# Kernel tuning notes

Hardware: AMD Instinct MI355X
Metric: run time of the kernel (lower is better)

The kernel has to match this reference:

```python
import jax, jax.numpy as jnp
import numpy as np

TOP_K = 8
NEG_SLOPE = 0.2  # PyG GATConv default negative_slope


def setup_inputs() -> dict:
    key = jax.random.key(0)
    ks = jax.random.split(key, 8)
    B, C, T, D, H, KD = 16, 64, 128, 256, 8, 32
    s = 1.0 / np.sqrt(D)
    return {
        "x": jax.random.normal(ks[0], (B, C, T, D), jnp.float32),
        "static_adj": jax.random.normal(ks[1], (C, C), jnp.float32),
        "w_q": jax.random.normal(ks[2], (KD, D), jnp.float32) * s,
        "w_k": jax.random.normal(ks[3], (KD, D), jnp.float32) * s,
        "gat_lin": jax.random.normal(ks[4], (H * D, D), jnp.float32) * s,  # shared lin_src/lin_dst
        "att_src": jax.random.normal(ks[5], (H, D), jnp.float32) * s,
        "att_dst": jax.random.normal(ks[6], (H, D), jnp.float32) * s,
        "gat_bias": jnp.zeros((D,), jnp.float32),
    }


def reference(x, static_adj, w_q, w_k, gat_lin, att_src, att_dst, gat_bias):
    B, C, T, D = x.shape
    H = att_src.shape[0]
    kd = w_q.shape[0]

    # ---- dynamic adjacency ----
    h = x.mean(axis=2)                                   # [B,C,D] temporal summary
    q = h @ w_q.T                                        # [B,C,KD]
    k = h @ w_k.T                                        # [B,C,KD]
    sim = jnp.einsum('bik,bjk->bij', q, k) / np.float32(np.sqrt(kd))
    delta_a = jnp.tanh(sim)                              # [B,C,C]
    adaptive = static_adj[None] + delta_a                # [B,C,C]

    # top-k per row -> sparse mask (edge: row i = source, col j = target, per dense_to_sparse)
    _, idx = jax.lax.top_k(jnp.abs(adaptive), TOP_K)     # [B,C,K]
    mask = jnp.any(jax.nn.one_hot(idx, C, dtype=bool), axis=-2)  # [B,C,C]
    mask = mask | jnp.eye(C, dtype=bool)                 # GATConv add_self_loops=True

    # ---- GAT message passing (dense masked attention, graph shared across T) ----
    xt = jnp.swapaxes(x, 1, 2)                           # [B,T,C,D]
    wx = (xt @ gat_lin.T).reshape(B, T, C, H, D)         # [B,T,C,H,F]
    a_s = jnp.einsum('btchf,hf->btch', wx, att_src)      # source term
    a_d = jnp.einsum('btchf,hf->btch', wx, att_dst)      # target term
    # e[b,t,i,j,h]: edge source i -> target j
    e = a_s[:, :, :, None, :] + a_d[:, :, None, :, :]
    e = jax.nn.leaky_relu(e, NEG_SLOPE)
    e = jnp.where(mask[:, None, :, :, None], e, -jnp.inf)
    alpha = jax.nn.softmax(e, axis=2)                    # softmax over incoming sources i per target j
    out = jnp.einsum('btijh,btihf->btjhf', alpha, wx)    # aggregate messages
    out = out.mean(axis=3) + gat_bias                    # concat=False -> mean heads, add bias
    x_updated = jnp.swapaxes(out, 1, 2)                  # [B,C,T,D]
    return x_updated, delta_a
```

## Files before the change

kernel.cpp:

```cpp
#include <hip/hip_runtime.h>

typedef _Float16 h2_t __attribute__((ext_vector_type(2)));
typedef _Float16 h4_t __attribute__((ext_vector_type(4)));
typedef _Float16 h8_t __attribute__((ext_vector_type(8)));
typedef __fp16 fp16x2 __attribute__((ext_vector_type(2)));
typedef float f32x16 __attribute__((ext_vector_type(16)));


__device__ __forceinline__ h2_t pkrtz(float a, float b) {
  union { fp16x2 f; h2_t h; } u;
  u.f = __builtin_amdgcn_cvt_pkrtz(a, b);
  return u.h;
}

__device__ __forceinline__ float fdot2_(h2_t a, h2_t b, float c) {
#if __has_builtin(__builtin_amdgcn_fdot2)
  return __builtin_amdgcn_fdot2(a, b, c, false);
#else
  return fmaf((float)a[0], (float)b[0], fmaf((float)a[1], (float)b[1], c));
#endif
}

__device__ __forceinline__ h2_t u2h(unsigned u) {
  union { unsigned u; h2_t h; } x; x.u = u; return x.h;
}

__device__ __forceinline__ void gload16(const void* g, void* l) {
  __builtin_amdgcn_global_load_lds(
      (const __attribute__((address_space(1))) void*)g,
      (__attribute__((address_space(3))) void*)l, 16, 0, 0);
}

__global__ void k_hmean(const float* __restrict__ x, float* __restrict__ h) {
  int bc = blockIdx.x;
  int d = threadIdx.x;
  const float* xp = x + (size_t)bc * (128 * 256) + d;
  float s = 0.f;
  #pragma unroll 8
  for (int t = 0; t < 128; ++t) s += xp[(size_t)t * 256];
  h[bc * 256 + d] = s * (1.f / 128.f);
}

__global__ void k_qk(const float* __restrict__ h, const float* __restrict__ wq,
                     const float* __restrict__ wk, float* __restrict__ q,
                     float* __restrict__ k) {
  int gid = blockIdx.x * 256 + threadIdx.x;
  int isK = gid >> 15;
  int e = gid & 32767;
  int kk = e & 31;
  int bi = e >> 5;
  const float4* h4 = (const float4*)(h + bi * 256);
  const float4* w4 = (const float4*)((isK ? wk : wq) + kk * 256);
  float s = 0.f;
  #pragma unroll 4
  for (int d = 0; d < 64; ++d) {
    float4 a = h4[d], bv = w4[d];
    s = fmaf(a.x, bv.x, s); s = fmaf(a.y, bv.y, s);
    s = fmaf(a.z, bv.z, s); s = fmaf(a.w, bv.w, s);
  }
  (isK ? k : q)[e] = s;
}

__global__ void k_adj(const float* __restrict__ q, const float* __restrict__ k,
                      const float* __restrict__ sadj, float* __restrict__ dout,
                      unsigned long long* __restrict__ cmask) {
  __shared__ float qs[64][33], ks[64][33];
  __shared__ float ad[64][65];
  __shared__ unsigned long long rowm[64];
  int b = blockIdx.x, tid = threadIdx.x;
  for (int r = 0; r < 8; ++r) {
    int idx = r * 256 + tid;
    qs[idx >> 5][idx & 31] = q[b * 2048 + idx];
    ks[idx >> 5][idx & 31] = k[b * 2048 + idx];
  }
  __syncthreads();
  const float rs = 0.17677669529663687f;
  for (int r = 0; r < 16; ++r) {
    int idx = r * 256 + tid;
    int i = idx >> 6, j = idx & 63;
    float s = 0.f;
    #pragma unroll 8
    for (int kk = 0; kk < 32; ++kk) s = fmaf(qs[i][kk], ks[j][kk], s);
    float dv = tanhf(s * rs);
    dout[b * 4096 + idx] = dv;
    ad[i][j] = sadj[idx] + dv;
  }
  __syncthreads();
  if (tid < 64) {
    unsigned long long sel = 0ull;
    for (int p = 0; p < 8; ++p) {
      float best = -1.f; int bj = 0;
      for (int j = 0; j < 64; ++j) {
        if ((sel >> j) & 1ull) continue;
        float v = fabsf(ad[tid][j]);
        if (v > best) { best = v; bj = j; }
      }
      sel |= 1ull << bj;
    }
    rowm[tid] = sel;
  }
  __syncthreads();
  if (tid < 64) {
    unsigned long long cmv = 1ull << tid;
    for (int i = 0; i < 64; ++i) cmv |= ((rowm[i] >> tid) & 1ull) << i;
    cmask[b * 64 + tid] = cmv;
  }
}

__global__ void k_vsd(const float* __restrict__ glin, const float* __restrict__ asrc,
                      const float* __restrict__ adst, _Float16* __restrict__ vsd16) {
  int hh = blockIdx.x, d = threadIdx.x;
  const float* gb = glin + (size_t)hh * 65536;
  float s = 0.f, t = 0.f;
  for (int f = 0; f < 256; ++f) {
    float g = gb[f * 256 + d];
    s = fmaf(asrc[hh * 256 + f], g, s);
    t = fmaf(adst[hh * 256 + f], g, t);
  }
  vsd16[hh * 256 + d] = (_Float16)s;
  vsd16[(8 + hh) * 256 + d] = (_Float16)t;
}

__global__ void k_gswz(const float* __restrict__ g, _Float16* __restrict__ o) {
  int gid = blockIdx.x * 256 + threadIdx.x;
  int s = gid & 7;
  int f = (gid >> 3) & 255;
  int sc = gid >> 11;
  int h = sc >> 2, dc = sc & 3;
  const float* src = g + ((size_t)(h * 256 + f) << 8) + dc * 64 + (((s ^ (f & 7)) & 7) << 3);
  float4 a = *(const float4*)src;
  float4 bq = *(const float4*)(src + 4);
  h8_t v;
  v[0] = (_Float16)a.x;  v[1] = (_Float16)a.y;  v[2] = (_Float16)a.z;  v[3] = (_Float16)a.w;
  v[4] = (_Float16)bq.x; v[5] = (_Float16)bq.y; v[6] = (_Float16)bq.z; v[7] = (_Float16)bq.w;
  *(h8_t*)(o + (size_t)gid * 8) = v;
}

__global__ __launch_bounds__(512) void k_main(
    const float* __restrict__ x, const _Float16* __restrict__ vsd16,
    const unsigned long long* __restrict__ cmask,
    const _Float16* __restrict__ g16s, const float* __restrict__ bias,
    float* __restrict__ out)
{
  __shared__ __align__(16) char LDS[143360];
  char* XR  = LDS;
  char* GB  = LDS + 32768;
  char* WXT = LDS + 98304;
  char* PT  = LDS + 131072;
  float* AS = (float*)(LDS + 139264);
  float* AD = (float*)(LDS + 141312);

  const int tid = threadIdx.x;
  const int lane = tid & 63;
  const int w = __builtin_amdgcn_readfirstlane(tid >> 6);
  const int hi = lane >> 5;
  const int l5 = lane & 31;
  const int l7 = lane & 7;
  const int mg = w & 1;
  const int fg = w >> 1;
  const int bt = blockIdx.x;
  const int b = bt >> 7, t = bt & 127;

  const int jj = w * 8 + (lane >> 3);
  const unsigned long long cm = cmask[b * 64 + jj];
  const int fb0 = l5 + fg * 64, fb1 = fb0 + 32;
  const float bi0 = bias[fb0], bi1 = bias[fb1];

  {
    const char* gs = (const char*)g16s + (size_t)w * 4096 + (size_t)lane * 16;
    char* ld = GB + w * 4096;
    #pragma unroll
    for (int q = 0; q < 4; ++q) gload16(gs + q * 1024, ld + q * 1024);
  }

  #pragma unroll
  for (int r = 0; r < 8; ++r) {
    int i = w * 8 + r;
    const float4 v = *(const float4*)(x + (((size_t)(b * 64 + i) * 128 + t) << 8) + lane * 4);
    h2_t p0 = pkrtz(v.x, v.y);
    h2_t p1 = pkrtz(v.z, v.w);
    h4_t hv; hv[0] = p0[0]; hv[1] = p0[1]; hv[2] = p1[0]; hv[3] = p1[1];
    int db = lane >> 1;
    int off = i * 512 + (((db & 24) | ((db ^ (i & 7)) & 7)) << 4) + ((lane & 1) << 3);
    *(h4_t*)(XR + off) = hv;
  }
  asm volatile("s_waitcnt vmcnt(0)" ::: "memory");
  asm volatile("s_waitcnt lgkmcnt(0)" ::: "memory");
  __builtin_amdgcn_s_barrier();

  h8_t Af[16];
  {
    int i = mg * 32 + l5;
    #pragma unroll
    for (int k = 0; k < 16; ++k) {
      int db = k * 2 + hi;
      Af[k] = *(const h8_t*)(XR + i * 512 + (((db & 24) | ((db ^ l7) & 7)) << 4));
    }
  }

  {
    float a_s = 0.f, a_d = 0.f;
    const unsigned* vsp = (const unsigned*)vsd16 + w * 128;
    const unsigned* vdp = (const unsigned*)vsd16 + (8 + w) * 128;
    #pragma unroll 4
    for (int db = 0; db < 32; ++db) {
      h8_t xv = *(const h8_t*)(XR + lane * 512 + (((db & 24) | ((db ^ l7) & 7)) << 4));
      #pragma unroll
      for (int c = 0; c < 4; ++c) {
        h2_t x2; x2[0] = xv[c * 2]; x2[1] = xv[c * 2 + 1];
        a_s = fdot2_(x2, u2h(vsp[db * 4 + c]), a_s);
        a_d = fdot2_(x2, u2h(vdp[db * 4 + c]), a_d);
      }
    }
    AS[w * 64 + lane] = a_s;
    AD[w * 64 + lane] = a_d;
  }
  asm volatile("s_waitcnt lgkmcnt(0)" ::: "memory");
  __builtin_amdgcn_s_barrier();

  f32x16 acc00 = {}, acc01 = {}, acc10 = {}, acc11 = {};

  #pragma unroll 1
  for (int h = 0; h < 8; ++h) {
    f32x16 d0 = {}, d1 = {};
    #pragma unroll
    for (int dc = 0; dc < 4; ++dc) {
      const int s = h * 4 + dc;
      asm volatile("s_waitcnt lgkmcnt(0)" ::: "memory");
      __builtin_amdgcn_s_barrier();
      if (s < 31) {
        const char* gs = (const char*)g16s + (size_t)(s + 1) * 32768 + (size_t)w * 4096 + (size_t)lane * 16;
        char* ld = GB + ((s + 1) & 1) * 32768 + w * 4096;
        #pragma unroll
        for (int q = 0; q < 4; ++q) gload16(gs + q * 1024, ld + q * 1024);
        asm volatile("s_waitcnt vmcnt(4)" ::: "memory");
      } else {
        asm volatile("s_waitcnt vmcnt(0)" ::: "memory");
      }
      __builtin_amdgcn_s_barrier();

      if (dc == 0) {
        const int ip = lane & 7;
        float ad_j = AD[h * 64 + jj];
        float ev[8], m = -1e30f;
        #pragma unroll
        for (int c = 0; c < 8; ++c) {
          int i = ip * 8 + c;
          float e = AS[h * 64 + i] + ad_j;
          e = (e > 0.f) ? e : 0.2f * e;
          e = ((cm >> i) & 1ULL) ? e : -1e30f;
          ev[c] = e; m = fmaxf(m, e);
        }
        m = fmaxf(m, __shfl_xor(m, 1));
        m = fmaxf(m, __shfl_xor(m, 2));
        m = fmaxf(m, __shfl_xor(m, 4));
        float ss = 0.f;
        #pragma unroll
        for (int c = 0; c < 8; ++c) { ev[c] = __expf(ev[c] - m); ss += ev[c]; }
        ss += __shfl_xor(ss, 1); ss += __shfl_xor(ss, 2); ss += __shfl_xor(ss, 4);
        float rinv = 1.f / ss;
        h8_t pv;
        #pragma unroll
        for (int c = 0; c < 4; ++c) {
          h2_t p = pkrtz(ev[2 * c] * rinv, ev[2 * c + 1] * rinv);
          pv[2 * c] = p[0]; pv[2 * c + 1] = p[1];
        }
        *(h8_t*)(PT + jj * 128 + (((ip ^ (jj & 7)) & 7) << 4)) = pv;
      }

      const char* gb = GB + (s & 1) * 32768;
      #pragma unroll
      for (int kk = 0; kk < 4; ++kk) {
        int sl = (((kk * 2 + hi) ^ l7) & 7) << 4;
        h8_t b0 = *(const h8_t*)(gb + fb0 * 128 + sl);
        h8_t b1 = *(const h8_t*)(gb + fb1 * 128 + sl);
        d0 = __builtin_amdgcn_mfma_f32_32x32x16_f16(Af[dc * 4 + kk], b0, d0, 0, 0, 0);
        d1 = __builtin_amdgcn_mfma_f32_32x32x16_f16(Af[dc * 4 + kk], b1, d1, 0, 0, 0);
      }
    }

    #pragma unroll
    for (int rq = 0; rq < 4; ++rq) {
      int db = mg * 4 + rq;
      int sl = ((db ^ l7) & 7) << 4;
      h2_t a0 = pkrtz(d0[rq * 4 + 0], d0[rq * 4 + 1]);
      h2_t a1 = pkrtz(d0[rq * 4 + 2], d0[rq * 4 + 3]);
      h4_t v0; v0[0] = a0[0]; v0[1] = a0[1]; v0[2] = a1[0]; v0[3] = a1[1];
      *(h4_t*)(WXT + fb0 * 128 + sl + hi * 8) = v0;
      h2_t b0p = pkrtz(d1[rq * 4 + 0], d1[rq * 4 + 1]);
      h2_t b1p = pkrtz(d1[rq * 4 + 2], d1[rq * 4 + 3]);
      h4_t v1; v1[0] = b0p[0]; v1[1] = b0p[1]; v1[2] = b1p[0]; v1[3] = b1p[1];
      *(h4_t*)(WXT + fb1 * 128 + sl + hi * 8) = v1;
    }
    asm volatile("s_waitcnt lgkmcnt(0)" ::: "memory");
    __builtin_amdgcn_s_barrier();

    #pragma unroll
    for (int kb = 0; kb < 4; ++kb) {
      int sl = (((kb * 2 + hi) ^ l7) & 7) << 4;
      h8_t pa0 = *(const h8_t*)(PT + l5 * 128 + sl);
      h8_t pa1 = *(const h8_t*)(PT + (l5 + 32) * 128 + sl);
      h8_t wb0 = *(const h8_t*)(WXT + fb0 * 128 + sl);
      h8_t wb1 = *(const h8_t*)(WXT + fb1 * 128 + sl);
      acc00 = __builtin_amdgcn_mfma_f32_32x32x16_f16(pa0, wb0, acc00, 0, 0, 0);
      acc01 = __builtin_amdgcn_mfma_f32_32x32x16_f16(pa0, wb1, acc01, 0, 0, 0);
      acc10 = __builtin_amdgcn_mfma_f32_32x32x16_f16(pa1, wb0, acc10, 0, 0, 0);
      acc11 = __builtin_amdgcn_mfma_f32_32x32x16_f16(pa1, wb1, acc11, 0, 0, 0);
    }
  }

  float* ob = out + ((size_t)(b * 64) * 128 + t) * 256;
  #pragma unroll
  for (int rq = 0; rq < 4; ++rq) {
    #pragma unroll
    for (int rr = 0; rr < 4; ++rr) {
      int r = rq * 4 + rr;
      int j0 = 8 * rq + 4 * hi + rr;
      ob[(size_t)j0 * 32768 + fb0]        = acc00[r] * 0.125f + bi0;
      ob[(size_t)j0 * 32768 + fb1]        = acc01[r] * 0.125f + bi1;
      ob[(size_t)(j0 + 32) * 32768 + fb0] = acc10[r] * 0.125f + bi0;
      ob[(size_t)(j0 + 32) * 32768 + fb1] = acc11[r] * 0.125f + bi1;
    }
  }
}

extern "C" void kernel_launch(void* const* d_in, const int* in_sizes, int n_in,
                              void* d_out, int out_size, void* d_ws, size_t ws_size,
                              hipStream_t stream) {
  const float* x    = (const float*)d_in[0];
  const float* sadj = (const float*)d_in[1];
  const float* wq   = (const float*)d_in[2];
  const float* wk   = (const float*)d_in[3];
  const float* glin = (const float*)d_in[4];
  const float* asrc = (const float*)d_in[5];
  const float* adst = (const float*)d_in[6];
  const float* bias = (const float*)d_in[7];

  float* out = (float*)d_out;
  float* delta_out = out + (size_t)16 * 64 * 128 * 256;

  char* ws = (char*)d_ws;
  float* h   = (float*)(ws + 0);
  float* q   = (float*)(ws + 1048576);
  float* k   = (float*)(ws + 1179648);
  unsigned long long* cm = (unsigned long long*)(ws + 1310720);
  _Float16* vsd16 = (_Float16*)(ws + 1318912);
  _Float16* g16s  = (_Float16*)(ws + 1327104);

  hipLaunchKernelGGL(k_hmean, dim3(1024), dim3(256), 0, stream, x, h);
  hipLaunchKernelGGL(k_qk,    dim3(256),  dim3(256), 0, stream, h, wq, wk, q, k);
  hipLaunchKernelGGL(k_adj,   dim3(16),   dim3(256), 0, stream, q, k, sadj, delta_out, cm);
  hipLaunchKernelGGL(k_vsd,   dim3(8),    dim3(256), 0, stream, glin, asrc, adst, vsd16);
  hipLaunchKernelGGL(k_gswz,  dim3(256),  dim3(256), 0, stream, glin, g16s);
  hipLaunchKernelGGL(k_main,  dim3(2048), dim3(512), 0, stream, x, vsd16, cm, g16s, bias, out);
}
```

Baseline: 373.4 us.

## Keep GAT weights and wx in registers, split aggregation K across wave pairs

Drops the LDS double-buffered weight staging. Each wave now loads pre-rearranged fp16 gat_lin fragments straight from global memory into registers, double-buffered as GA/GB. The wx tile is repacked in registers through lane shuffles instead of a round trip through LDS, and the softmax is precomputed once per (head, target) as a log-sum-exp offset, so attention weights are built directly in registers. The aggregation K dimension is split across the two mg wave groups and combined through an LDS reduction at the end. This removes most per-step barriers and cuts LDS use, in exchange for more register pressure and redundant global weight loads per wave.

Result: slower. 419.0 us (+12.2%).

```diff
diff --git a/kernel.cpp b/kernel.cpp
--- a/kernel.cpp
+++ b/kernel.cpp
@@ -11,6 +11,18 @@
   union { fp16x2 f; h2_t h; } u;
   u.f = __builtin_amdgcn_cvt_pkrtz(a, b);
   return u.h;
+}
+
+__device__ __forceinline__ unsigned pk_u(float a, float b) {
+  union { fp16x2 f; unsigned u; } z;
+  z.f = __builtin_amdgcn_cvt_pkrtz(a, b);
+  return z.u;
+}
+
+__device__ __forceinline__ h8_t mk8(unsigned w0, unsigned w1, unsigned w2, unsigned w3) {
+  union { unsigned u[4]; h8_t h; } z;
+  z.u[0] = w0; z.u[1] = w1; z.u[2] = w2; z.u[3] = w3;
+  return z.h;
 }
 
 __device__ __forceinline__ float fdot2_(h2_t a, h2_t b, float c) {
@@ -23,12 +35,6 @@
 
 __device__ __forceinline__ h2_t u2h(unsigned u) {
   union { unsigned u; h2_t h; } x; x.u = u; return x.h;
-}
-
-__device__ __forceinline__ void gload16(const void* g, void* l) {
-  __builtin_amdgcn_global_load_lds(
-      (const __attribute__((address_space(1))) void*)g,
-      (__attribute__((address_space(3))) void*)l, 16, 0, 0);
 }
 
 __global__ void k_hmean(const float* __restrict__ x, float* __restrict__ h) {
@@ -121,13 +127,17 @@
   vsd16[(8 + hh) * 256 + d] = (_Float16)t;
 }
 
-__global__ void k_gswz(const float* __restrict__ g, _Float16* __restrict__ o) {
+__global__ void k_grearr(const float* __restrict__ g, _Float16* __restrict__ o) {
   int gid = blockIdx.x * 256 + threadIdx.x;
-  int s = gid & 7;
-  int f = (gid >> 3) & 255;
-  int sc = gid >> 11;
-  int h = sc >> 2, dc = sc & 3;
-  const float* src = g + ((size_t)(h * 256 + f) << 8) + dc * 64 + (((s ^ (f & 7)) & 7) << 3);
+  int lane = gid & 63;
+  int fg = (gid >> 6) & 3;
+  int FID = gid >> 8;
+  int ft = FID & 1, kk = (FID >> 1) & 3, s = FID >> 3;
+  int h = s >> 2, dc = s & 3;
+  int l5 = lane & 31, hi = lane >> 5;
+  int f = fg * 64 + ft * 32 + l5;
+  int d0 = dc * 64 + kk * 16 + hi * 8;
+  const float* src = g + ((size_t)(h * 256 + f) << 8) + d0;
   float4 a = *(const float4*)src;
   float4 bq = *(const float4*)(src + 4);
   h8_t v;
@@ -139,16 +149,15 @@
 __global__ __launch_bounds__(512) void k_main(
     const float* __restrict__ x, const _Float16* __restrict__ vsd16,
     const unsigned long long* __restrict__ cmask,
-    const _Float16* __restrict__ g16s, const float* __restrict__ bias,
+    const _Float16* __restrict__ g16r, const float* __restrict__ bias,
     float* __restrict__ out)
 {
-  __shared__ __align__(16) char LDS[143360];
-  char* XR  = LDS;
-  char* GB  = LDS + 32768;
-  char* WXT = LDS + 98304;
-  char* PT  = LDS + 131072;
-  float* AS = (float*)(LDS + 139264);
-  float* AD = (float*)(LDS + 141312);
+  __shared__ __align__(16) char LDS[106496];
+  char* XR   = LDS;
+  float* ASp = (float*)(LDS + 32768);
+  float* ADp = (float*)(LDS + 34816);
+  float* OFFp= (float*)(LDS + 36864);
+  char* RED  = LDS + 40960;
 
   const int tid = threadIdx.x;
   const int lane = tid & 63;
@@ -161,17 +170,19 @@
   const int bt = blockIdx.x;
   const int b = bt >> 7, t = bt & 127;
 
-  const int jj = w * 8 + (lane >> 3);
-  const unsigned long long cm = cmask[b * 64 + jj];
-  const int fb0 = l5 + fg * 64, fb1 = fb0 + 32;
-  const float bi0 = bias[fb0], bi1 = bias[fb1];
-
-  {
-    const char* gs = (const char*)g16s + (size_t)w * 4096 + (size_t)lane * 16;
-    char* ld = GB + w * 4096;
-    #pragma unroll
-    for (int q = 0; q < 4; ++q) gload16(gs + q * 1024, ld + q * 1024);
-  }
+  const char* gb0 = (const char*)g16r + fg * 1024 + lane * 16;
+
+  h8_t GA[8], GB[8];
+  #pragma unroll
+  for (int q = 0; q < 8; ++q) GA[q] = *(const h8_t*)(gb0 + q * 4096);
+
+  const unsigned long long cm0 = cmask[b * 64 + l5];
+  const unsigned long long cm1 = cmask[b * 64 + 32 + l5];
+  const int shb = mg * 32 + hi * 8;
+  const unsigned mb00 = (unsigned)(cm0 >> shb)        & 0xffu;
+  const unsigned mb01 = (unsigned)(cm0 >> (shb + 16)) & 0xffu;
+  const unsigned mb10 = (unsigned)(cm1 >> shb)        & 0xffu;
+  const unsigned mb11 = (unsigned)(cm1 >> (shb + 16)) & 0xffu;
 
   #pragma unroll
   for (int r = 0; r < 8; ++r) {
@@ -184,9 +195,7 @@
     int off = i * 512 + (((db & 24) | ((db ^ (i & 7)) & 7)) << 4) + ((lane & 1) << 3);
     *(h4_t*)(XR + off) = hv;
   }
-  asm volatile("s_waitcnt vmcnt(0)" ::: "memory");
-  asm volatile("s_waitcnt lgkmcnt(0)" ::: "memory");
-  __builtin_amdgcn_s_barrier();
+  __syncthreads();
 
   h8_t Af[16];
   {
@@ -212,115 +221,174 @@
         a_d = fdot2_(x2, u2h(vdp[db * 4 + c]), a_d);
       }
     }
-    AS[w * 64 + lane] = a_s;
-    AD[w * 64 + lane] = a_d;
+    ASp[w * 64 + lane] = a_s;
+    ADp[w * 64 + lane] = a_d;
   }
   asm volatile("s_waitcnt lgkmcnt(0)" ::: "memory");
-  __builtin_amdgcn_s_barrier();
+
+  {
+    const int j = lane;
+    const unsigned long long cmj = cmask[b * 64 + j];
+    const float adj = ADp[w * 64 + j];
+    float m = -1e30f;
+    #pragma unroll 8
+    for (int i = 0; i < 64; ++i) {
+      float e = ASp[w * 64 + i] + adj;
+      e = fmaxf(e, 0.f) + 0.2f * fminf(e, 0.f);
+      e = ((cmj >> i) & 1ull) ? e : -1e30f;
+      m = fmaxf(m, e);
+    }
+    float ssum = 0.f;
+    #pragma unroll 8
+    for (int i = 0; i < 64; ++i) {
+      float e = ASp[w * 64 + i] + adj;
+      e = fmaxf(e, 0.f) + 0.2f * fminf(e, 0.f);
+      e = ((cmj >> i) & 1ull) ? e : -1e30f;
+      ssum += exp2f((e - m) * 1.44269504f);
+    }
+    OFFp[w * 64 + j] = fmaf(-1.44269504f, m, -log2f(ssum));
+  }
+  __syncthreads();
 
   f32x16 acc00 = {}, acc01 = {}, acc10 = {}, acc11 = {};
 
   #pragma unroll 1
   for (int h = 0; h < 8; ++h) {
     f32x16 d0 = {}, d1 = {};
+
     #pragma unroll
     for (int dc = 0; dc < 4; ++dc) {
       const int s = h * 4 + dc;
-      asm volatile("s_waitcnt lgkmcnt(0)" ::: "memory");
-      __builtin_amdgcn_s_barrier();
-      if (s < 31) {
-        const char* gs = (const char*)g16s + (size_t)(s + 1) * 32768 + (size_t)w * 4096 + (size_t)lane * 16;
-        char* ld = GB + ((s + 1) & 1) * 32768 + w * 4096;
-        #pragma unroll
-        for (int q = 0; q < 4; ++q) gload16(gs + q * 1024, ld + q * 1024);
-        asm volatile("s_waitcnt vmcnt(4)" ::: "memory");
+      const int sp = (s < 31) ? s + 1 : 31;
+      const char* gpp = gb0 + (size_t)sp * 32768;
+      if ((dc & 1) == 0) {
+        #pragma unroll
+        for (int q = 0; q < 8; ++q) GB[q] = *(const h8_t*)(gpp + q * 4096);
+        #pragma unroll
+        for (int kk = 0; kk < 4; ++kk) {
+          d0 = __builtin_amdgcn_mfma_f32_32x32x16_f16(Af[dc * 4 + kk], GA[kk * 2 + 0], d0, 0, 0, 0);
+          d1 = __builtin_amdgcn_mfma_f32_32x32x16_f16(Af[dc * 4 + kk], GA[kk * 2 + 1], d1, 0, 0, 0);
+        }
       } else {
-        asm volatile("s_waitcnt vmcnt(0)" ::: "memory");
-      }
-      __builtin_amdgcn_s_barrier();
-
-      if (dc == 0) {
-        const int ip = lane & 7;
-        float ad_j = AD[h * 64 + jj];
-        float ev[8], m = -1e30f;
-        #pragma unroll
-        for (int c = 0; c < 8; ++c) {
-          int i = ip * 8 + c;
-          float e = AS[h * 64 + i] + ad_j;
-          e = (e > 0.f) ? e : 0.2f * e;
-          e = ((cm >> i) & 1ULL) ? e : -1e30f;
-          ev[c] = e; m = fmaxf(m, e);
-        }
-        m = fmaxf(m, __shfl_xor(m, 1));
-        m = fmaxf(m, __shfl_xor(m, 2));
-        m = fmaxf(m, __shfl_xor(m, 4));
-        float ss = 0.f;
-        #pragma unroll
-        for (int c = 0; c < 8; ++c) { ev[c] = __expf(ev[c] - m); ss += ev[c]; }
-        ss += __shfl_xor(ss, 1); ss += __shfl_xor(ss, 2); ss += __shfl_xor(ss, 4);
-        float rinv = 1.f / ss;
-        h8_t pv;
-        #pragma unroll
-        for (int c = 0; c < 4; ++c) {
-          h2_t p = pkrtz(ev[2 * c] * rinv, ev[2 * c + 1] * rinv);
-          pv[2 * c] = p[0]; pv[2 * c + 1] = p[1];
-        }
-        *(h8_t*)(PT + jj * 128 + (((ip ^ (jj & 7)) & 7) << 4)) = pv;
-      }
-
-      const char* gb = GB + (s & 1) * 32768;
+        #pragma unroll
+        for (int q = 0; q < 8; ++q) GA[q] = *(const h8_t*)(gpp + q * 4096);
+        #pragma unroll
+        for (int kk = 0; kk < 4; ++kk) {
+          d0 = __builtin_amdgcn_mfma_f32_32x32x16_f16(Af[dc * 4 + kk], GB[kk * 2 + 0], d0, 0, 0, 0);
+          d1 = __builtin_amdgcn_mfma_f32_32x32x16_f16(Af[dc * 4 + kk], GB[kk * 2 + 1], d1, 0, 0, 0);
+        }
+      }
+    }
+
+    h8_t B2[2][2];
+    {
+      const bool H = (hi != 0);
       #pragma unroll
-      for (int kk = 0; kk < 4; ++kk) {
-        int sl = (((kk * 2 + hi) ^ l7) & 7) << 4;
-        h8_t b0 = *(const h8_t*)(gb + fb0 * 128 + sl);
-        h8_t b1 = *(const h8_t*)(gb + fb1 * 128 + sl);
-        d0 = __builtin_amdgcn_mfma_f32_32x32x16_f16(Af[dc * 4 + kk], b0, d0, 0, 0, 0);
-        d1 = __builtin_amdgcn_mfma_f32_32x32x16_f16(Af[dc * 4 + kk], b1, d1, 0, 0, 0);
-      }
-    }
-
+      for (int ft = 0; ft < 2; ++ft) {
+        const f32x16& dd = ft ? d1 : d0;
+        unsigned P0 = pk_u(dd[0], dd[1]),  P1 = pk_u(dd[2], dd[3]);
+        unsigned P2 = pk_u(dd[4], dd[5]),  P3 = pk_u(dd[6], dd[7]);
+        unsigned P4 = pk_u(dd[8], dd[9]),  P5 = pk_u(dd[10], dd[11]);
+        unsigned P6 = pk_u(dd[12], dd[13]), P7 = pk_u(dd[14], dd[15]);
+        {
+          unsigned Pa = H ? P2 : P0, Pb = H ? P3 : P1;
+          unsigned Qa = H ? P0 : P2, Qb = H ? P1 : P3;
+          unsigned S0 = (unsigned)__shfl_xor((int)Qa, 32);
+          unsigned S1 = (unsigned)__shfl_xor((int)Qb, 32);
+          B2[0][ft] = mk8(H ? S0 : Pa, H ? S1 : Pb, H ? Pa : S0, H ? Pb : S1);
+        }
+        {
+          unsigned Pa = H ? P6 : P4, Pb = H ? P7 : P5;
+          unsigned Qa = H ? P4 : P6, Qb = H ? P5 : P7;
+          unsigned S0 = (unsigned)__shfl_xor((int)Qa, 32);
+          unsigned S1 = (unsigned)__shfl_xor((int)Qb, 32);
+          B2[1][ft] = mk8(H ? S0 : Pa, H ? S1 : Pb, H ? Pa : S0, H ? Pb : S1);
+        }
+      }
+    }
+
+    const float adj0 = ADp[h * 64 + l5];
+    const float adj1 = ADp[h * 64 + 32 + l5];
+    const float off0 = OFFp[h * 64 + l5];
+    const float off1 = OFFp[h * 64 + 32 + l5];
+    const float* asp = ASp + h * 64 + mg * 32 + hi * 8;
+    float4 asA0 = *(const float4*)(asp);
+    float4 asA1 = *(const float4*)(asp + 4);
+    float4 asB0 = *(const float4*)(asp + 16);
+    float4 asB1 = *(const float4*)(asp + 20);
+    float asv[2][8];
+    asv[0][0]=asA0.x; asv[0][1]=asA0.y; asv[0][2]=asA0.z; asv[0][3]=asA0.w;
+    asv[0][4]=asA1.x; asv[0][5]=asA1.y; asv[0][6]=asA1.z; asv[0][7]=asA1.w;
+    asv[1][0]=asB0.x; asv[1][1]=asB0.y; asv[1][2]=asB0.z; asv[1][3]=asB0.w;
+    asv[1][4]=asB1.x; asv[1][5]=asB1.y; asv[1][6]=asB1.z; asv[1][7]=asB1.w;
+
+    h8_t A2[2][2];
     #pragma unroll
-    for (int rq = 0; rq < 4; ++rq) {
-      int db = mg * 4 + rq;
-      int sl = ((db ^ l7) & 7) << 4;
-      h2_t a0 = pkrtz(d0[rq * 4 + 0], d0[rq * 4 + 1]);
-      h2_t a1 = pkrtz(d0[rq * 4 + 2], d0[rq * 4 + 3]);
-      h4_t v0; v0[0] = a0[0]; v0[1] = a0[1]; v0[2] = a1[0]; v0[3] = a1[1];
-      *(h4_t*)(WXT + fb0 * 128 + sl + hi * 8) = v0;
-      h2_t b0p = pkrtz(d1[rq * 4 + 0], d1[rq * 4 + 1]);
-      h2_t b1p = pkrtz(d1[rq * 4 + 2], d1[rq * 4 + 3]);
-      h4_t v1; v1[0] = b0p[0]; v1[1] = b0p[1]; v1[2] = b1p[0]; v1[3] = b1p[1];
-      *(h4_t*)(WXT + fb1 * 128 + sl + hi * 8) = v1;
-    }
-    asm volatile("s_waitcnt lgkmcnt(0)" ::: "memory");
-    __builtin_amdgcn_s_barrier();
-
+    for (int jt = 0; jt < 2; ++jt) {
+      const float adj = jt ? adj1 : adj0;
+      const float off = jt ? off1 : off0;
+      #pragma unroll
+      for (int kbl = 0; kbl < 2; ++kbl) {
+        const unsigned mb = jt ? (kbl ? mb11 : mb10) : (kbl ? mb01 : mb00);
+        float vv[8];
+        #pragma unroll
+        for (int e = 0; e < 8; ++e) {
+          float ee = asv[kbl][e] + adj;
+          ee = fmaxf(ee, 0.f) + 0.2f * fminf(ee, 0.f);
+          ee = ((mb >> e) & 1u) ? ee : -1e30f;
+          vv[e] = exp2f(fmaf(ee, 1.44269504f, off));
+        }
+        A2[jt][kbl] = mk8(pk_u(vv[0], vv[1]), pk_u(vv[2], vv[3]),
+                          pk_u(vv[4], vv[5]), pk_u(vv[6], vv[7]));
+      }
+    }
+
+    acc00 = __builtin_amdgcn_mfma_f32_32x32x16_f16(A2[0][0], B2[0][0], acc00, 0, 0, 0);
+    acc00 = __builtin_amdgcn_mfma_f32_32x32x16_f16(A2[0][1], B2[1][0], acc00, 0, 0, 0);
+    acc01 = __builtin_amdgcn_mfma_f32_32x32x16_f16(A2[0][0], B2[0][1], acc01, 0, 0, 0);
+    acc01 = __builtin_amdgcn_mfma_f32_32x32x16_f16(A2[0][1], B2[1][1], acc01, 0, 0, 0);
+    acc10 = __builtin_amdgcn_mfma_f32_32x32x16_f16(A2[1][0], B2[0][0], acc10, 0, 0, 0);
+    acc10 = __builtin_amdgcn_mfma_f32_32x32x16_f16(A2[1][1], B2[1][0], acc10, 0, 0, 0);
+    acc11 = __builtin_amdgcn_mfma_f32_32x32x16_f16(A2[1][0], B2[0][1], acc11, 0, 0, 0);
+    acc11 = __builtin_amdgcn_mfma_f32_32x32x16_f16(A2[1][1], B2[1][1], acc11, 0, 0, 0);
+  }
+
+  if (mg == 1) {
     #pragma unroll
-    for (int kb = 0; kb < 4; ++kb) {
-      int sl = (((kb * 2 + hi) ^ l7) & 7) << 4;
-      h8_t pa0 = *(const h8_t*)(PT + l5 * 128 + sl);
-      h8_t pa1 = *(const h8_t*)(PT + (l5 + 32) * 128 + sl);
-      h8_t wb0 = *(const h8_t*)(WXT + fb0 * 128 + sl);
-      h8_t wb1 = *(const h8_t*)(WXT + fb1 * 128 + sl);
-      acc00 = __builtin_amdgcn_mfma_f32_32x32x16_f16(pa0, wb0, acc00, 0, 0, 0);
-      acc01 = __builtin_amdgcn_mfma_f32_32x32x16_f16(pa0, wb1, acc01, 0, 0, 0);
-      acc10 = __builtin_amdgcn_mfma_f32_32x32x16_f16(pa1, wb0, acc10, 0, 0, 0);
-      acc11 = __builtin_amdgcn_mfma_f32_32x32x16_f16(pa1, wb1, acc11, 0, 0, 0);
-    }
-  }
-
-  float* ob = out + ((size_t)(b * 64) * 128 + t) * 256;
-  #pragma unroll
-  for (int rq = 0; rq < 4; ++rq) {
+    for (int jt = 0; jt < 2; ++jt)
+      #pragma unroll
+      for (int ft = 0; ft < 2; ++ft) {
+        const f32x16& a = jt ? (ft ? acc11 : acc10) : (ft ? acc01 : acc00);
+        #pragma unroll
+        for (int rq = 0; rq < 4; ++rq) {
+          float4 v; v.x = a[rq*4+0]; v.y = a[rq*4+1]; v.z = a[rq*4+2]; v.w = a[rq*4+3];
+          *(float4*)(RED + (((((fg*2+jt)*2+ft)*4 + rq)*64 + lane) << 4)) = v;
+        }
+      }
+  }
+  __syncthreads();
+  if (mg == 0) {
+    const float bi0 = bias[fg * 64 + l5];
+    const float bi1 = bias[fg * 64 + 32 + l5];
+    float* ob = out + ((size_t)(b * 64) * 128 + t) * 256;
     #pragma unroll
-    for (int rr = 0; rr < 4; ++rr) {
-      int r = rq * 4 + rr;
-      int j0 = 8 * rq + 4 * hi + rr;
-      ob[(size_t)j0 * 32768 + fb0]        = acc00[r] * 0.125f + bi0;
-      ob[(size_t)j0 * 32768 + fb1]        = acc01[r] * 0.125f + bi1;
-      ob[(size_t)(j0 + 32) * 32768 + fb0] = acc10[r] * 0.125f + bi0;
-      ob[(size_t)(j0 + 32) * 32768 + fb1] = acc11[r] * 0.125f + bi1;
-    }
+    for (int jt = 0; jt < 2; ++jt)
+      #pragma unroll
+      for (int ft = 0; ft < 2; ++ft) {
+        const f32x16& a = jt ? (ft ? acc11 : acc10) : (ft ? acc01 : acc00);
+        const float bv = ft ? bi1 : bi0;
+        const int fcol = fg * 64 + ft * 32 + l5;
+        #pragma unroll
+        for (int rq = 0; rq < 4; ++rq) {
+          float4 p = *(const float4*)(RED + (((((fg*2+jt)*2+ft)*4 + rq)*64 + lane) << 4));
+          #pragma unroll
+          for (int rr = 0; rr < 4; ++rr) {
+            int j = jt * 32 + rr + 8 * rq + 4 * hi;
+            float sum = a[rq*4+rr] + ((const float*)&p)[rr];
+            ob[(size_t)j * 32768 + fcol] = sum * 0.125f + bv;
+          }
+        }
+      }
   }
 }
 
@@ -345,12 +413,12 @@
   float* k   = (float*)(ws + 1179648);
   unsigned long long* cm = (unsigned long long*)(ws + 1310720);
   _Float16* vsd16 = (_Float16*)(ws + 1318912);
-  _Float16* g16s  = (_Float16*)(ws + 1327104);
-
-  hipLaunchKernelGGL(k_hmean, dim3(1024), dim3(256), 0, stream, x, h);
-  hipLaunchKernelGGL(k_qk,    dim3(256),  dim3(256), 0, stream, h, wq, wk, q, k);
-  hipLaunchKernelGGL(k_adj,   dim3(16),   dim3(256), 0, stream, q, k, sadj, delta_out, cm);
-  hipLaunchKernelGGL(k_vsd,   dim3(8),    dim3(256), 0, stream, glin, asrc, adst, vsd16);
-  hipLaunchKernelGGL(k_gswz,  dim3(256),  dim3(256), 0, stream, glin, g16s);
-  hipLaunchKernelGGL(k_main,  dim3(2048), dim3(512), 0, stream, x, vsd16, cm, g16s, bias, out);
-}
+  _Float16* g16r  = (_Float16*)(ws + 1327104);
+
+  hipLaunchKernelGGL(k_hmean,  dim3(1024), dim3(256), 0, stream, x, h);
+  hipLaunchKernelGGL(k_qk,     dim3(256),  dim3(256), 0, stream, h, wq, wk, q, k);
+  hipLaunchKernelGGL(k_adj,    dim3(16),   dim3(256), 0, stream, q, k, sadj, delta_out, cm);
+  hipLaunchKernelGGL(k_vsd,    dim3(8),    dim3(256), 0, stream, glin, asrc, adst, vsd16);
+  hipLaunchKernelGGL(k_grearr, dim3(256),  dim3(256), 0, stream, glin, g16r);
+  hipLaunchKernelGGL(k_main,   dim3(2048), dim3(512), 0, stream, x, vsd16, cm, g16r, bias, out);
+}
```
